# Performance work log

Measured on AMD Instinct MI355X. Metric: run time of the kernel, lower is better.

## Reference

```python
import jax, jax.numpy as jnp
import numpy as np

K = 3
STRIDE = 1
PAD = 1
C_IN = 256
C_OUT = 256
BN_EPS = 1e-5


def conv2d(x, w, b, stride, pad):
    # x: (N,C,H,W), w: (O,I,K,K)
    y = jax.lax.conv_general_dilated(
        x, w, window_strides=(stride, stride),
        padding=((pad, pad), (pad, pad)),
        dimension_numbers=("NCHW", "OIHW", "NCHW"))
    return y + b[None, :, None, None]


def deform_conv2d(x, offset, weight, stride, pad, k):
    # torchvision-style deformable conv v1 (no modulation, no bias),
    # offset layout: (N, 2*k*k, Ho, Wo) with (dy, dx) pairs per kernel tap.
    N, C, H, W = x.shape
    Ho, Wo = offset.shape[2], offset.shape[3]
    KK = k * k
    off = offset.reshape(N, KK, 2, Ho, Wo)
    dy, dx = off[:, :, 0], off[:, :, 1]                      # (N,KK,Ho,Wo)

    ky, kx = jnp.meshgrid(jnp.arange(k), jnp.arange(k), indexing="ij")
    ky = ky.reshape(1, KK, 1, 1).astype(x.dtype)
    kx = kx.reshape(1, KK, 1, 1).astype(x.dtype)
    base_y = (jnp.arange(Ho) * stride - pad).astype(x.dtype)[None, None, :, None]
    base_x = (jnp.arange(Wo) * stride - pad).astype(x.dtype)[None, None, None, :]

    py = base_y + ky + dy                                     # (N,KK,Ho,Wo)
    px = base_x + kx + dx

    y0 = jnp.floor(py)
    x0 = jnp.floor(px)
    ly = py - y0
    lx = px - x0
    y0i = y0.astype(jnp.int32)
    x0i = x0.astype(jnp.int32)

    x_flat = x.reshape(N, C, H * W)

    def gather(yi, xi):
        valid = (yi >= 0) & (yi < H) & (xi >= 0) & (xi < W)
        yc = jnp.clip(yi, 0, H - 1)
        xc = jnp.clip(xi, 0, W - 1)
        idx = yc * W + xc                                     # (N,KK,Ho,Wo)
        v = jax.vmap(lambda xf, i: xf[:, i])(x_flat, idx)     # (N,C,KK,Ho,Wo)
        return v * valid[:, None].astype(x.dtype)

    w_tl = ((1 - ly) * (1 - lx))[:, None]
    w_tr = ((1 - ly) * lx)[:, None]
    w_bl = (ly * (1 - lx))[:, None]
    w_br = (ly * lx)[:, None]

    val = (w_tl * gather(y0i, x0i) + w_tr * gather(y0i, x0i + 1)
           + w_bl * gather(y0i + 1, x0i) + w_br * gather(y0i + 1, x0i + 1))
    # val: (N, Ci, KK, Ho, Wo); weight: (Co, Ci, k, k)
    w2 = weight.reshape(weight.shape[0], weight.shape[1], KK)
    return jnp.einsum("bikhw,oik->bohw", val, w2)


def setup_inputs() -> dict:
    key = jax.random.key(0)
    k1, k2, k3, k4 = jax.random.split(key, 4)
    N, H, W = 8, 64, 64
    x = jax.random.normal(k1, (N, C_IN, H, W), dtype=jnp.float32)
    # small nonzero offset-conv weights so the deformable gather is exercised
    w_offset = jax.random.normal(k2, (2 * K * K, C_IN, K, K), dtype=jnp.float32) * 0.01
    b_offset = jax.random.normal(k3, (2 * K * K,), dtype=jnp.float32) * 0.1
    w_conv = jax.random.normal(k4, (C_OUT, C_IN, K, K), dtype=jnp.float32) / np.sqrt(C_IN * K * K)
    gamma = jnp.ones((C_OUT,), dtype=jnp.float32)
    beta = jnp.zeros((C_OUT,), dtype=jnp.float32)
    return {"x": x, "w_offset": w_offset, "b_offset": b_offset,
            "w_conv": w_conv, "gamma": gamma, "beta": beta}


def reference(x, w_offset, b_offset, w_conv, gamma, beta):
    offset = conv2d(x, w_offset, b_offset, STRIDE, PAD)
    out = deform_conv2d(x, offset, w_conv, STRIDE, PAD, K)
    # BatchNorm2d in training mode: batch stats over (N,H,W), biased variance
    mean = jnp.mean(out, axis=(0, 2, 3), keepdims=True)
    var = jnp.mean(jnp.square(out - mean), axis=(0, 2, 3), keepdims=True)
    out = (out - mean) * jax.lax.rsqrt(var + BN_EPS)
    out = out * gamma[None, :, None, None] + beta[None, :, None, None]
    return out * jax.nn.sigmoid(out)  # SiLU
```

## Files before the change

kernel.cpp:

```cpp
#include <hip/hip_runtime.h>
#include <math.h>

#define HW 4096
#define KTOT 2304

typedef __attribute__((ext_vector_type(8))) short short8v;
typedef __attribute__((ext_vector_type(4))) float float4v;

__device__ __forceinline__ unsigned int bf16rne(float f) {
  unsigned int x = __float_as_uint(f);
  return (x + 0x7fffu + ((x >> 16) & 1u)) >> 16;
}

__device__ __forceinline__ unsigned int bilin_pack(unsigned int u0, unsigned int u1,
                                                   unsigned int u2, unsigned int u3,
                                                   float w0, float w1, float w2, float w3) {
  float lo = w0 * __uint_as_float(u0 << 16) + w1 * __uint_as_float(u1 << 16) +
             w2 * __uint_as_float(u2 << 16) + w3 * __uint_as_float(u3 << 16);
  float hi = w0 * __uint_as_float(u0 & 0xFFFF0000u) + w1 * __uint_as_float(u1 & 0xFFFF0000u) +
             w2 * __uint_as_float(u2 & 0xFFFF0000u) + w3 * __uint_as_float(u3 & 0xFFFF0000u);
  unsigned int r;
  asm("v_cvt_pk_bf16_f32 %0, %1, %2" : "=v"(r) : "v"(lo), "v"(hi));
  return r;
}


__global__ __launch_bounds__(256) void k_tx(const float* __restrict__ x,
                                            ushort* __restrict__ xT) {
  int bid = blockIdx.x;
  int n = bid & 7, p0 = (bid >> 3) << 6;
  int t = threadIdx.x;
  int lane = t & 63, wave = t >> 6, c0 = wave << 6;
  const float* xb = x + ((size_t)(n * 256 + c0)) * HW + p0 + lane;
  ushort* ob = xT + ((size_t)n * 4096 + p0 + lane) * 256 + c0;
#pragma unroll
  for (int g = 0; g < 8; ++g) {
    unsigned int u[4];
#pragma unroll
    for (int j = 0; j < 4; ++j) {
      float v0 = xb[(size_t)(g * 8 + 2 * j) * HW];
      float v1 = xb[(size_t)(g * 8 + 2 * j + 1) * HW];
      u[j] = bf16rne(v0) | (bf16rne(v1) << 16);
    }
    *reinterpret_cast<uint4*>(ob + g * 8) = make_uint4(u[0], u[1], u[2], u[3]);
  }
}

__global__ __launch_bounds__(256) void k_prep(const float* __restrict__ wc,
                                              const float* __restrict__ wo,
                                              ushort* __restrict__ wB,
                                              ushort* __restrict__ wOB) {
  int bid = blockIdx.x;
  if (bid < 288) {
    int t = bid * 256 + threadIdx.x;
    int ks = t >> 10;
    int l = t & 63;
    int of = (t >> 6) & 15;
    int kk = ks >> 3;
    int cbase = ((ks & 7) << 5) + ((l >> 4) << 3);
    int oc = (of << 4) + (l & 15);
    unsigned int u[8];
#pragma unroll
    for (int j = 0; j < 8; ++j)
      u[j] = bf16rne(wc[(size_t)oc * KTOT + (size_t)(cbase + j) * 9 + kk]);
    *reinterpret_cast<uint4*>(&wB[(size_t)t * 8]) =
        make_uint4(u[0] | (u[1] << 16), u[2] | (u[3] << 16),
                   u[4] | (u[5] << 16), u[6] | (u[7] << 16));
  } else {
    int t = (bid - 288) * 256 + threadIdx.x;
    int ks = t >> 7;
    int l = t & 63;
    int of = (t >> 6) & 1;
    int kk = ks >> 3;
    int cbase = ((ks & 7) << 5) + ((l >> 4) << 3);
    int oc = (of << 4) + (l & 15);
    unsigned int u[8];
#pragma unroll
    for (int j = 0; j < 8; ++j)
      u[j] = (oc < 18) ? bf16rne(wo[(size_t)oc * KTOT + (size_t)(cbase + j) * 9 + kk]) : 0u;
    *reinterpret_cast<uint4*>(&wOB[(size_t)t * 8]) =
        make_uint4(u[0] | (u[1] << 16), u[2] | (u[3] << 16),
                   u[4] | (u[5] << 16), u[6] | (u[7] << 16));
  }
}

__global__ __launch_bounds__(256, 2) void k_offset4(
    const ushort* __restrict__ xT, const ushort* __restrict__ wOffB,
    const float* __restrict__ b_off, float* __restrict__ off_out) {
  __shared__ ushort s_tile[2][64 * 64];

  int bid = blockIdx.x;
  int n = bid & 7, ho = bid >> 3;
  int t = threadIdx.x;
  int lane = t & 63, wave = t >> 6;
  int pp = lane >> 3, coct = lane & 7;
  int q0 = (wave << 3) + pp;
  int q1 = q0 + 32;

  const ushort* xTn = xT + (size_t)n * 4096 * 256;

  float4v acc[2];
  acc[0] = (float4v)0.f;
  acc[1] = (float4v)0.f;

  auto srcs = [&](int kk, const ushort*& s0, const ushort*& s1, bool& v0, bool& v1) {
    int ky = kk / 3, kx = kk - ky * 3;
    int oy = ho + ky - 1;
    int ox0 = q0 + kx - 1, ox1 = q1 + kx - 1;
    bool okY = (oy >= 0) & (oy < 64);
    v0 = okY & (ox0 >= 0) & (ox0 < 64);
    v1 = okY & (ox1 >= 0) & (ox1 < 64);
    s0 = xTn + (size_t)(oy * 64 + ox0) * 256 + (coct << 3);
    s1 = xTn + (size_t)(oy * 64 + ox1) * 256 + (coct << 3);
  };

  auto issue = [&](uint4& a, uint4& b, const ushort* s0, const ushort* s1,
                   bool v0, bool v1, int cg) {
    a = v0 ? *reinterpret_cast<const uint4*>(s0 + (cg << 6)) : make_uint4(0, 0, 0, 0);
    b = v1 ? *reinterpret_cast<const uint4*>(s1 + (cg << 6)) : make_uint4(0, 0, 0, 0);
  };

  auto step = [&](uint4 a, uint4 b, int ksb, int buf) {
    short8v wf[2][2];
#pragma unroll
    for (int ks2 = 0; ks2 < 2; ++ks2)
#pragma unroll
      for (int of = 0; of < 2; ++of)
        wf[ks2][of] = *reinterpret_cast<const short8v*>(
            &wOffB[(((size_t)((ksb + ks2) * 2 + of)) * 64 + lane) * 8]);
    *reinterpret_cast<uint4*>(&s_tile[buf][q0 * 64 + ((coct ^ pp) << 3)]) = a;
    *reinterpret_cast<uint4*>(&s_tile[buf][q1 * 64 + ((coct ^ pp) << 3)]) = b;
    asm volatile("s_waitcnt lgkmcnt(0)" ::: "memory");
    __builtin_amdgcn_s_barrier();
#pragma unroll
    for (int ks2 = 0; ks2 < 2; ++ks2) {
      int row = (wave << 4) + (lane & 15);
      int g = (ks2 << 2) + (lane >> 4);
      int slot = g ^ (row & 7);
      short8v vf = *reinterpret_cast<const short8v*>(&s_tile[buf][row * 64 + slot * 8]);
      acc[0] = __builtin_amdgcn_mfma_f32_16x16x32_bf16(wf[ks2][0], vf, acc[0], 0, 0, 0);
      acc[1] = __builtin_amdgcn_mfma_f32_16x16x32_bf16(wf[ks2][1], vf, acc[1], 0, 0, 0);
    }
  };

  const ushort *cs0, *cs1;
  bool cv0, cv1;
  srcs(0, cs0, cs1, cv0, cv1);
  uint4 A0, A1, B0, B1;
  issue(A0, A1, cs0, cs1, cv0, cv1, 0);

  for (int kk = 0; kk < 9; ++kk) {
    int ksb = kk << 3;
    issue(B0, B1, cs0, cs1, cv0, cv1, 1);
    step(A0, A1, ksb + 0, 0);
    issue(A0, A1, cs0, cs1, cv0, cv1, 2);
    step(B0, B1, ksb + 2, 1);
    issue(B0, B1, cs0, cs1, cv0, cv1, 3);
    step(A0, A1, ksb + 4, 0);
    const ushort *ns0 = cs0, *ns1 = cs1;
    bool nv0 = cv0, nv1 = cv1;
    if (kk < 8) {
      srcs(kk + 1, ns0, ns1, nv0, nv1);
      issue(A0, A1, ns0, ns1, nv0, nv1, 0);
    }
    step(B0, B1, ksb + 6, 1);
    cs0 = ns0; cs1 = ns1; cv0 = nv0; cv1 = nv1;
  }

  int pixcol = (wave << 4) + (lane & 15);
  size_t base = ((size_t)n * 4096 + ho * 64 + pixcol) * 18;
#pragma unroll
  for (int of = 0; of < 2; ++of)
#pragma unroll
    for (int j = 0; j < 4; ++j) {
      int oc = (of << 4) + ((lane >> 4) << 2) + j;
      if (oc < 18) off_out[base + oc] = acc[of][j] + b_off[oc];
    }
}

__global__ __launch_bounds__(512, 4) void k_deform7(
    const ushort* __restrict__ xT, const float* __restrict__ off,
    const ushort* __restrict__ wB, float* __restrict__ out,
    float2* __restrict__ part) {
  __shared__ ushort s_val[2][64 * 64];
  __shared__ int4   s_gi[9][64];
  __shared__ float4 s_gw[9][64];

  int bid = blockIdx.x;
  int n = bid & 7, ho = bid >> 3;
  int t = threadIdx.x;
  int lane = t & 63, wave = t >> 6;
  int coct = lane & 7;
  int p = (wave << 3) + (lane >> 3);

  const ushort* xTn = xT + (size_t)n * 4096 * 256;

  for (int e = t; e < 576; e += 512) {
    int pix = e & 63, kk = e >> 6;
    int ky = kk / 3, kx = kk - ky * 3;
    const float* ob = off + ((size_t)n * 4096 + ho * 64 + pix) * 18;
    float dy = ob[2 * kk], dx = ob[2 * kk + 1];
    float py = (float)(ho - 1 + ky) + dy;
    float px = (float)(pix - 1 + kx) + dx;
    float y0f = floorf(py), x0f = floorf(px);
    float ly = py - y0f, lx = px - x0f;
    int y0 = (int)y0f, x0 = (int)x0f;
    int y1 = y0 + 1, x1 = x0 + 1;
    float vy0 = (y0 >= 0 && y0 < 64) ? 1.f : 0.f;
    float vy1 = (y1 >= 0 && y1 < 64) ? 1.f : 0.f;
    float vx0 = (x0 >= 0 && x0 < 64) ? 1.f : 0.f;
    float vx1 = (x1 >= 0 && x1 < 64) ? 1.f : 0.f;
    int cy0 = min(max(y0, 0), 63) << 6, cy1 = min(max(y1, 0), 63) << 6;
    int cx0 = min(max(x0, 0), 63), cx1 = min(max(x1, 0), 63);
    s_gi[kk][pix] = make_int4((cy0 + cx0) << 8, (cy0 + cx1) << 8,
                              (cy1 + cx0) << 8, (cy1 + cx1) << 8);
    s_gw[kk][pix] = make_float4((1.f - ly) * (1.f - lx) * vy0 * vx0,
                                (1.f - ly) * lx * vy0 * vx1,
                                ly * (1.f - lx) * vy1 * vx0,
                                ly * lx * vy1 * vx1);
  }
  __syncthreads();

  float4v acc[2][4];
#pragma unroll
  for (int a = 0; a < 2; ++a)
#pragma unroll
    for (int b = 0; b < 4; ++b) acc[a][b] = (float4v)0.f;

  uint4 TA[4], TB[4];

  auto issue = [&](uint4 (&T)[4], int kk, int cg) {
    int4 g = s_gi[kk][p];
    int cb = (cg << 6) + (coct << 3);
    T[0] = *reinterpret_cast<const uint4*>(xTn + g.x + cb);
    T[1] = *reinterpret_cast<const uint4*>(xTn + g.y + cb);
    T[2] = *reinterpret_cast<const uint4*>(xTn + g.z + cb);
    T[3] = *reinterpret_cast<const uint4*>(xTn + g.w + cb);
  };

  auto step = [&](uint4 (&T)[4], int kk, int ks0, int buf) {
    short8v wf[2][2];
#pragma unroll
    for (int ks2 = 0; ks2 < 2; ++ks2)
#pragma unroll
      for (int mf = 0; mf < 2; ++mf)
        wf[ks2][mf] = *reinterpret_cast<const short8v*>(
            &wB[(((size_t)((ks0 + ks2) * 16 + (wave << 1) + mf)) * 64 + lane) * 8]);
    float4 w = s_gw[kk][p];
    uint4 r;
    r.x = bilin_pack(T[0].x, T[1].x, T[2].x, T[3].x, w.x, w.y, w.z, w.w);
    r.y = bilin_pack(T[0].y, T[1].y, T[2].y, T[3].y, w.x, w.y, w.z, w.w);
    r.z = bilin_pack(T[0].z, T[1].z, T[2].z, T[3].z, w.x, w.y, w.z, w.w);
    r.w = bilin_pack(T[0].w, T[1].w, T[2].w, T[3].w, w.x, w.y, w.z, w.w);
    *reinterpret_cast<uint4*>(&s_val[buf][p * 64 + ((coct ^ (p & 7)) << 3)]) = r;
    asm volatile("s_waitcnt lgkmcnt(0)" ::: "memory");
    __builtin_amdgcn_s_barrier();
#pragma unroll
    for (int ks2 = 0; ks2 < 2; ++ks2) {
#pragma unroll
      for (int pf = 0; pf < 4; ++pf) {
        int row = (pf << 4) + (lane & 15);
        int g = (ks2 << 2) + (lane >> 4);
        int slot = g ^ (row & 7);
        short8v vf = *reinterpret_cast<const short8v*>(&s_val[buf][row * 64 + slot * 8]);
#pragma unroll
        for (int mf = 0; mf < 2; ++mf)
          acc[mf][pf] = __builtin_amdgcn_mfma_f32_16x16x32_bf16(
              wf[ks2][mf], vf, acc[mf][pf], 0, 0, 0);
      }
    }
  };

  issue(TA, 0, 0);
  for (int kk = 0; kk < 9; ++kk) {
    int ks0 = kk << 3;
    issue(TB, kk, 1);
    step(TA, kk, ks0 + 0, 0);
    issue(TA, kk, 2);
    step(TB, kk, ks0 + 2, 1);
    issue(TB, kk, 3);
    step(TA, kk, ks0 + 4, 0);
    if (kk < 8) issue(TA, kk + 1, 0);
    step(TB, kk, ks0 + 6, 1);
  }

#pragma unroll
  for (int mf = 0; mf < 2; ++mf) {
    int ocb = (wave << 5) + (mf << 4) + ((lane >> 4) << 2);
#pragma unroll
    for (int pf = 0; pf < 4; ++pf) {
      int wo = (pf << 4) + (lane & 15);
      float* op = out + (((size_t)(n * 256 + ocb)) * 64 + ho) * 64 + wo;
      float4v a = acc[mf][pf];
      op[0] = a[0];
      op[HW] = a[1];
      op[2 * HW] = a[2];
      op[3 * HW] = a[3];
    }
  }
  float s[2][4], q[2][4];
#pragma unroll
  for (int mf = 0; mf < 2; ++mf)
#pragma unroll
    for (int j = 0; j < 4; ++j) {
      float ss = 0.f, qq = 0.f;
#pragma unroll
      for (int pf = 0; pf < 4; ++pf) {
        float v = acc[mf][pf][j];
        ss += v;
        qq += v * v;
      }
      s[mf][j] = ss;
      q[mf][j] = qq;
    }
#pragma unroll
  for (int o = 1; o < 16; o <<= 1) {
#pragma unroll
    for (int mf = 0; mf < 2; ++mf)
#pragma unroll
      for (int j = 0; j < 4; ++j) {
        s[mf][j] += __shfl_xor(s[mf][j], o);
        q[mf][j] += __shfl_xor(q[mf][j], o);
      }
  }
  if ((lane & 15) == 0) {
#pragma unroll
    for (int mf = 0; mf < 2; ++mf)
#pragma unroll
      for (int j = 0; j < 4; ++j) {
        int oc = (wave << 5) + (mf << 4) + ((lane >> 4) << 2) + j;
        part[(size_t)oc * 512 + bid] = make_float2(s[mf][j], q[mf][j]);
      }
  }
}

__global__ __launch_bounds__(256) void k_stats_fin(const float2* __restrict__ part,
                                                   float2* __restrict__ stats) {
  int oc = blockIdx.x;
  int t = threadIdx.x;
  float2 a = part[(size_t)oc * 512 + t];
  float2 b = part[(size_t)oc * 512 + 256 + t];
  float s = a.x + b.x, q = a.y + b.y;
#pragma unroll
  for (int o = 32; o; o >>= 1) {
    s += __shfl_down(s, o);
    q += __shfl_down(q, o);
  }
  __shared__ float2 wsum[4];
  if ((t & 63) == 0) wsum[t >> 6] = make_float2(s, q);
  __syncthreads();
  if (t == 0) {
    float S = wsum[0].x + wsum[1].x + wsum[2].x + wsum[3].x;
    float Q = wsum[0].y + wsum[1].y + wsum[2].y + wsum[3].y;
    float mean = S / 32768.f;
    float var = Q / 32768.f - mean * mean;
    stats[oc] = make_float2(mean, rsqrtf(var + 1e-5f));
  }
}

__global__ __launch_bounds__(256) void k_bn_silu(float* __restrict__ out,
                                                 const float2* __restrict__ stats,
                                                 const float* __restrict__ gamma,
                                                 const float* __restrict__ beta) {
  int b = blockIdx.x;
  int nb = (b & 7) * 1024 + (b >> 3);
  size_t i4 = (size_t)nb * 256 + threadIdx.x;
  int ch = (int)((i4 >> 10) & 255);
  float2 st = stats[ch];
  float g = gamma[ch] * st.y;
  float bb = beta[ch] - st.x * g;
  float4 v = *(float4*)(out + i4 * 4);
  float y0 = v.x * g + bb, y1 = v.y * g + bb, y2 = v.z * g + bb, y3 = v.w * g + bb;
  v.x = y0 / (1.f + expf(-y0));
  v.y = y1 / (1.f + expf(-y1));
  v.z = y2 / (1.f + expf(-y2));
  v.w = y3 / (1.f + expf(-y3));
  *(float4*)(out + i4 * 4) = v;
}

extern "C" void kernel_launch(void* const* d_in, const int* in_sizes, int n_in,
                              void* d_out, int out_size, void* d_ws, size_t ws_size,
                              hipStream_t stream) {
  const float* x      = (const float*)d_in[0];
  const float* w_off  = (const float*)d_in[1];
  const float* b_off  = (const float*)d_in[2];
  const float* w_conv = (const float*)d_in[3];
  const float* gamma  = (const float*)d_in[4];
  const float* beta   = (const float*)d_in[5];
  float* out = (float*)d_out;

  float* ws       = (float*)d_ws;
  float*  ws_off  = ws;
  ushort* ws_xT   = (ushort*)(ws + 589824);
  ushort* ws_wB   = (ushort*)(ws + 4784128);
  ushort* ws_wOB  = (ushort*)(ws + 5079040);
  float2* ws_part = (float2*)(ws + 5115904);
  float2* ws_st   = (float2*)(ws + 5378048);

  k_tx<<<512, 256, 0, stream>>>(x, ws_xT);
  k_prep<<<324, 256, 0, stream>>>(w_conv, w_off, ws_wB, ws_wOB);
  k_offset4<<<512, 256, 0, stream>>>(ws_xT, ws_wOB, b_off, ws_off);
  k_deform7<<<512, 512, 0, stream>>>(ws_xT, ws_off, ws_wB, out, ws_part);
  k_stats_fin<<<256, 256, 0, stream>>>(ws_part, ws_st);
  k_bn_silu<<<8192, 256, 0, stream>>>(out, ws_st, gamma, beta);
}
```

Measured before the change: 109.7 us.

## Merge transpose/prep kernels, widen offset conv blocks, raise MFMA wave priority

Folds the x transpose and the weight prep into one launch with block-range dispatch, which removes a kernel launch. The offset conv now runs 512 threads per block: each wave loads a single pixel row and splits the output-channel and pixel fragments across waves, giving more waves per block and fewer registers per thread. The deform kernel raises wave priority with s_setprio around the MFMA section so matrix work is favoured over other waves' gathers. Risks: heavier barrier contention in the offset kernel, and priority changes that may not help scheduling.

```diff
diff --git a/kernel.cpp b/kernel.cpp
--- a/kernel.cpp
+++ b/kernel.cpp
@@ -25,34 +25,32 @@
 }
 
 
-__global__ __launch_bounds__(256) void k_tx(const float* __restrict__ x,
-                                            ushort* __restrict__ xT) {
+__global__ __launch_bounds__(256) void k_tx_prep(const float* __restrict__ x,
+                                                 const float* __restrict__ wc,
+                                                 const float* __restrict__ wo,
+                                                 ushort* __restrict__ xT,
+                                                 ushort* __restrict__ wB,
+                                                 ushort* __restrict__ wOB) {
   int bid = blockIdx.x;
-  int n = bid & 7, p0 = (bid >> 3) << 6;
-  int t = threadIdx.x;
-  int lane = t & 63, wave = t >> 6, c0 = wave << 6;
-  const float* xb = x + ((size_t)(n * 256 + c0)) * HW + p0 + lane;
-  ushort* ob = xT + ((size_t)n * 4096 + p0 + lane) * 256 + c0;
-#pragma unroll
-  for (int g = 0; g < 8; ++g) {
-    unsigned int u[4];
-#pragma unroll
-    for (int j = 0; j < 4; ++j) {
-      float v0 = xb[(size_t)(g * 8 + 2 * j) * HW];
-      float v1 = xb[(size_t)(g * 8 + 2 * j + 1) * HW];
-      u[j] = bf16rne(v0) | (bf16rne(v1) << 16);
-    }
-    *reinterpret_cast<uint4*>(ob + g * 8) = make_uint4(u[0], u[1], u[2], u[3]);
-  }
-}
-
-__global__ __launch_bounds__(256) void k_prep(const float* __restrict__ wc,
-                                              const float* __restrict__ wo,
-                                              ushort* __restrict__ wB,
-                                              ushort* __restrict__ wOB) {
-  int bid = blockIdx.x;
-  if (bid < 288) {
-    int t = bid * 256 + threadIdx.x;
+  if (bid < 512) {
+    int n = bid & 7, p0 = (bid >> 3) << 6;
+    int t = threadIdx.x;
+    int lane = t & 63, wave = t >> 6, c0 = wave << 6;
+    const float* xb = x + ((size_t)(n * 256 + c0)) * HW + p0 + lane;
+    ushort* ob = xT + ((size_t)n * 4096 + p0 + lane) * 256 + c0;
+#pragma unroll
+    for (int g = 0; g < 8; ++g) {
+      unsigned int u[4];
+#pragma unroll
+      for (int j = 0; j < 4; ++j) {
+        float v0 = xb[(size_t)(g * 8 + 2 * j) * HW];
+        float v1 = xb[(size_t)(g * 8 + 2 * j + 1) * HW];
+        u[j] = bf16rne(v0) | (bf16rne(v1) << 16);
+      }
+      *reinterpret_cast<uint4*>(ob + g * 8) = make_uint4(u[0], u[1], u[2], u[3]);
+    }
+  } else if (bid < 800) {
+    int t = (bid - 512) * 256 + threadIdx.x;
     int ks = t >> 10;
     int l = t & 63;
     int of = (t >> 6) & 15;
@@ -67,7 +65,7 @@
         make_uint4(u[0] | (u[1] << 16), u[2] | (u[3] << 16),
                    u[4] | (u[5] << 16), u[6] | (u[7] << 16));
   } else {
-    int t = (bid - 288) * 256 + threadIdx.x;
+    int t = (bid - 800) * 256 + threadIdx.x;
     int ks = t >> 7;
     int l = t & 63;
     int of = (t >> 6) & 1;
@@ -84,7 +82,7 @@
   }
 }
 
-__global__ __launch_bounds__(256, 2) void k_offset4(
+__global__ __launch_bounds__(512, 4) void k_offset5(
     const ushort* __restrict__ xT, const ushort* __restrict__ wOffB,
     const float* __restrict__ b_off, float* __restrict__ off_out) {
   __shared__ ushort s_tile[2][64 * 64];
@@ -93,92 +91,78 @@
   int n = bid & 7, ho = bid >> 3;
   int t = threadIdx.x;
   int lane = t & 63, wave = t >> 6;
-  int pp = lane >> 3, coct = lane & 7;
-  int q0 = (wave << 3) + pp;
-  int q1 = q0 + 32;
+  int coct = lane & 7;
+  int p = (wave << 3) + (lane >> 3);
+  int ocf = wave & 1, pixf = wave >> 1;
 
   const ushort* xTn = xT + (size_t)n * 4096 * 256;
 
-  float4v acc[2];
-  acc[0] = (float4v)0.f;
-  acc[1] = (float4v)0.f;
-
-  auto srcs = [&](int kk, const ushort*& s0, const ushort*& s1, bool& v0, bool& v1) {
+  float4v acc = (float4v)0.f;
+
+  auto srcp = [&](int kk, const ushort*& s, bool& v) {
     int ky = kk / 3, kx = kk - ky * 3;
-    int oy = ho + ky - 1;
-    int ox0 = q0 + kx - 1, ox1 = q1 + kx - 1;
-    bool okY = (oy >= 0) & (oy < 64);
-    v0 = okY & (ox0 >= 0) & (ox0 < 64);
-    v1 = okY & (ox1 >= 0) & (ox1 < 64);
-    s0 = xTn + (size_t)(oy * 64 + ox0) * 256 + (coct << 3);
-    s1 = xTn + (size_t)(oy * 64 + ox1) * 256 + (coct << 3);
-  };
-
-  auto issue = [&](uint4& a, uint4& b, const ushort* s0, const ushort* s1,
-                   bool v0, bool v1, int cg) {
-    a = v0 ? *reinterpret_cast<const uint4*>(s0 + (cg << 6)) : make_uint4(0, 0, 0, 0);
-    b = v1 ? *reinterpret_cast<const uint4*>(s1 + (cg << 6)) : make_uint4(0, 0, 0, 0);
-  };
-
-  auto step = [&](uint4 a, uint4 b, int ksb, int buf) {
-    short8v wf[2][2];
+    int oy = ho + ky - 1, ox = p + kx - 1;
+    v = (oy >= 0) & (oy < 64) & (ox >= 0) & (ox < 64);
+    s = xTn + (size_t)(oy * 64 + ox) * 256 + (coct << 3);
+  };
+
+  auto issue = [&](uint4& a, const ushort* s, bool v, int cg) {
+    a = v ? *reinterpret_cast<const uint4*>(s + (cg << 6)) : make_uint4(0, 0, 0, 0);
+  };
+
+  auto step = [&](uint4 a, int ksb, int buf) {
+    short8v wf[2];
 #pragma unroll
     for (int ks2 = 0; ks2 < 2; ++ks2)
-#pragma unroll
-      for (int of = 0; of < 2; ++of)
-        wf[ks2][of] = *reinterpret_cast<const short8v*>(
-            &wOffB[(((size_t)((ksb + ks2) * 2 + of)) * 64 + lane) * 8]);
-    *reinterpret_cast<uint4*>(&s_tile[buf][q0 * 64 + ((coct ^ pp) << 3)]) = a;
-    *reinterpret_cast<uint4*>(&s_tile[buf][q1 * 64 + ((coct ^ pp) << 3)]) = b;
+      wf[ks2] = *reinterpret_cast<const short8v*>(
+          &wOffB[(((size_t)((ksb + ks2) * 2 + ocf)) * 64 + lane) * 8]);
+    *reinterpret_cast<uint4*>(&s_tile[buf][p * 64 + ((coct ^ (p & 7)) << 3)]) = a;
     asm volatile("s_waitcnt lgkmcnt(0)" ::: "memory");
     __builtin_amdgcn_s_barrier();
 #pragma unroll
     for (int ks2 = 0; ks2 < 2; ++ks2) {
-      int row = (wave << 4) + (lane & 15);
+      int row = (pixf << 4) + (lane & 15);
       int g = (ks2 << 2) + (lane >> 4);
       int slot = g ^ (row & 7);
       short8v vf = *reinterpret_cast<const short8v*>(&s_tile[buf][row * 64 + slot * 8]);
-      acc[0] = __builtin_amdgcn_mfma_f32_16x16x32_bf16(wf[ks2][0], vf, acc[0], 0, 0, 0);
-      acc[1] = __builtin_amdgcn_mfma_f32_16x16x32_bf16(wf[ks2][1], vf, acc[1], 0, 0, 0);
-    }
-  };
-
-  const ushort *cs0, *cs1;
-  bool cv0, cv1;
-  srcs(0, cs0, cs1, cv0, cv1);
-  uint4 A0, A1, B0, B1;
-  issue(A0, A1, cs0, cs1, cv0, cv1, 0);
+      acc = __builtin_amdgcn_mfma_f32_16x16x32_bf16(wf[ks2], vf, acc, 0, 0, 0);
+    }
+  };
+
+  const ushort* cs;
+  bool cv;
+  srcp(0, cs, cv);
+  uint4 A, B;
+  issue(A, cs, cv, 0);
 
   for (int kk = 0; kk < 9; ++kk) {
     int ksb = kk << 3;
-    issue(B0, B1, cs0, cs1, cv0, cv1, 1);
-    step(A0, A1, ksb + 0, 0);
-    issue(A0, A1, cs0, cs1, cv0, cv1, 2);
-    step(B0, B1, ksb + 2, 1);
-    issue(B0, B1, cs0, cs1, cv0, cv1, 3);
-    step(A0, A1, ksb + 4, 0);
-    const ushort *ns0 = cs0, *ns1 = cs1;
-    bool nv0 = cv0, nv1 = cv1;
+    issue(B, cs, cv, 1);
+    step(A, ksb + 0, 0);
+    issue(A, cs, cv, 2);
+    step(B, ksb + 2, 1);
+    issue(B, cs, cv, 3);
+    step(A, ksb + 4, 0);
+    const ushort* ns = cs;
+    bool nv = cv;
     if (kk < 8) {
-      srcs(kk + 1, ns0, ns1, nv0, nv1);
-      issue(A0, A1, ns0, ns1, nv0, nv1, 0);
-    }
-    step(B0, B1, ksb + 6, 1);
-    cs0 = ns0; cs1 = ns1; cv0 = nv0; cv1 = nv1;
-  }
-
-  int pixcol = (wave << 4) + (lane & 15);
+      srcp(kk + 1, ns, nv);
+      issue(A, ns, nv, 0);
+    }
+    step(B, ksb + 6, 1);
+    cs = ns; cv = nv;
+  }
+
+  int pixcol = (pixf << 4) + (lane & 15);
   size_t base = ((size_t)n * 4096 + ho * 64 + pixcol) * 18;
 #pragma unroll
-  for (int of = 0; of < 2; ++of)
-#pragma unroll
-    for (int j = 0; j < 4; ++j) {
-      int oc = (of << 4) + ((lane >> 4) << 2) + j;
-      if (oc < 18) off_out[base + oc] = acc[of][j] + b_off[oc];
-    }
-}
-
-__global__ __launch_bounds__(512, 4) void k_deform7(
+  for (int j = 0; j < 4; ++j) {
+    int oc = (ocf << 4) + ((lane >> 4) << 2) + j;
+    if (oc < 18) off_out[base + oc] = acc[j] + b_off[oc];
+  }
+}
+
+__global__ __launch_bounds__(512, 4) void k_deform10(
     const ushort* __restrict__ xT, const float* __restrict__ off,
     const ushort* __restrict__ wB, float* __restrict__ out,
     float2* __restrict__ part) {
@@ -255,6 +239,7 @@
     *reinterpret_cast<uint4*>(&s_val[buf][p * 64 + ((coct ^ (p & 7)) << 3)]) = r;
     asm volatile("s_waitcnt lgkmcnt(0)" ::: "memory");
     __builtin_amdgcn_s_barrier();
+    __builtin_amdgcn_s_setprio(1);
 #pragma unroll
     for (int ks2 = 0; ks2 < 2; ++ks2) {
 #pragma unroll
@@ -269,6 +254,7 @@
               wf[ks2][mf], vf, acc[mf][pf], 0, 0, 0);
       }
     }
+    __builtin_amdgcn_s_setprio(0);
   };
 
   issue(TA, 0, 0);
@@ -397,10 +383,9 @@
   float2* ws_part = (float2*)(ws + 5115904);
   float2* ws_st   = (float2*)(ws + 5378048);
 
-  k_tx<<<512, 256, 0, stream>>>(x, ws_xT);
-  k_prep<<<324, 256, 0, stream>>>(w_conv, w_off, ws_wB, ws_wOB);
-  k_offset4<<<512, 256, 0, stream>>>(ws_xT, ws_wOB, b_off, ws_off);
-  k_deform7<<<512, 512, 0, stream>>>(ws_xT, ws_off, ws_wB, out, ws_part);
+  k_tx_prep<<<836, 256, 0, stream>>>(x, w_conv, w_off, ws_xT, ws_wB, ws_wOB);
+  k_offset5<<<512, 512, 0, stream>>>(ws_xT, ws_wOB, b_off, ws_off);
+  k_deform10<<<512, 512, 0, stream>>>(ws_xT, ws_off, ws_wB, out, ws_part);
   k_stats_fin<<<256, 256, 0, stream>>>(ws_part, ws_st);
   k_bn_silu<<<8192, 256, 0, stream>>>(out, ws_st, gamma, beta);
 }
```

Result: no change. 108.4 us (-1.2%).
